# Kernel tuning notes

Measured on AMD Instinct MI355X. Metric: run time of the kernel, lower is better.

Reference implementation:

```python
import jax, jax.numpy as jnp
import numpy as np
import math

B, S, D, H = 2, 2048, 1024, 16
DK = D // H
THETA = 10000.0

def _rope_tables(seq_len, dk, theta):
    freqs = 1.0 / theta ** (np.arange(0, dk, 2)[: dk // 2].astype(np.float32) / dk)
    t = np.arange(seq_len, dtype=np.float32)
    ang = np.outer(t, freqs)  # [S, dk/2]
    return jnp.asarray(np.cos(ang)), jnp.asarray(np.sin(ang))

def setup_inputs() -> dict:
    key = jax.random.key(0)
    ks = jax.random.split(key, 12)
    init = lambda k, shape: (0.02 * jax.random.normal(k, shape)).astype(jnp.float32)
    cos, sin = _rope_tables(S, DK, THETA)
    mask = jnp.tril(jnp.ones((S, S), dtype=jnp.int32))[None, None]  # [1,1,S,S] causal
    return {
        'Q': jax.random.normal(ks[0], (B, S, D), jnp.float32),
        'K': jax.random.normal(ks[1], (B, S, D), jnp.float32),
        'V': jax.random.normal(ks[2], (B, S, D), jnp.float32),
        'mask': mask,
        'Wq_w': init(ks[3], (D, D)), 'Wq_b': init(ks[4], (D,)),
        'Wk_w': init(ks[5], (D, D)), 'Wk_b': init(ks[6], (D,)),
        'Wv_w': init(ks[7], (D, D)), 'Wv_b': init(ks[8], (D,)),
        'Wo_w': init(ks[9], (D, D)), 'Wo_b': init(ks[10], (D,)),
        'cos': cos, 'sin': sin,
    }

def _apply_rope(x, cos, sin):
    # x: [B, S, H, DK]; cos/sin: [S, DK/2]
    x1 = x[..., 0::2]
    x2 = x[..., 1::2]
    c = cos[None, :, None, :]
    s = sin[None, :, None, :]
    out_even = x1 * c - x2 * s
    out_odd = x1 * s + x2 * c
    return jnp.stack([out_even, out_odd], axis=-1).reshape(x.shape)

def reference(Q, K, V, mask, Wq_w, Wq_b, Wk_w, Wk_b, Wv_w, Wv_b, Wo_w, Wo_b, cos, sin):
    b, s, d = Q.shape
    q = (Q @ Wq_w.T + Wq_b).reshape(b, s, H, DK)
    k = (K @ Wk_w.T + Wk_b).reshape(b, s, H, DK)
    v = (V @ Wv_w.T + Wv_b).reshape(b, s, H, DK)
    q = _apply_rope(q, cos[:s], sin[:s])
    k = _apply_rope(k, cos[:s], sin[:s])
    # [B,H,S,DK]
    q = q.transpose(0, 2, 1, 3)
    k = k.transpose(0, 2, 1, 3)
    v = v.transpose(0, 2, 1, 3)
    scores = jnp.einsum('bhqd,bhkd->bhqk', q, k) / math.sqrt(DK)
    scores = jnp.where(mask == 0, jnp.float32(-1e9), scores)
    probs = jax.nn.softmax(scores, axis=-1)
    out = jnp.einsum('bhqk,bhkd->bhqd', probs, v)  # [B,H,S,DK]
    out = out.transpose(0, 2, 1, 3).reshape(b, s, d)
    return out @ Wo_w.T + Wo_b
```

## Files before the change

kernel.cpp:

```cpp
#include <hip/hip_runtime.h>
#include <cstdint>
#include <cstddef>


typedef __bf16 bf16x8 __attribute__((ext_vector_type(8)));
typedef float floatx4 __attribute__((ext_vector_type(4)));

#define DI __device__ __forceinline__

DI unsigned short f2bf(float f) {
  union { float f; unsigned int u; } v; v.f = f;
  unsigned int r = v.u + 0x7fffu + ((v.u >> 16) & 1u);
  return (unsigned short)(r >> 16);
}

DI unsigned short bfb(float f) {
  __bf16 h = (__bf16)f;
  union { __bf16 h; unsigned short u; } c; c.h = h;
  return c.u;
}

DI void gld16(const void* g, void* l) {
  __builtin_amdgcn_global_load_lds(
      (const __attribute__((address_space(1))) void*)g,
      (__attribute__((address_space(3))) void*)l, 16, 0, 0);
}

__global__ void cvt_all(const float* __restrict__ Q, const float* __restrict__ K,
                        const float* __restrict__ V, const float* __restrict__ Wq,
                        const float* __restrict__ Wk, const float* __restrict__ Wv,
                        const float* __restrict__ Wo, unsigned short* __restrict__ dst) {
  int i = blockIdx.x * blockDim.x + threadIdx.x;
  const float* s;
  int off;
  if (i < 3145728) {
    if (i < 1048576) { s = Q; off = i; }
    else if (i < 2097152) { s = K; off = i - 1048576; }
    else { s = V; off = i - 2097152; }
  } else {
    int j = i - 3145728;
    int wsel = j >> 18;
    off = j & 262143;
    s = (wsel == 0) ? Wq : (wsel == 1) ? Wk : (wsel == 2) ? Wv : Wo;
  }
  float4 f = reinterpret_cast<const float4*>(s)[off];
  ushort4 o;
  o.x = f2bf(f.x); o.y = f2bf(f.y); o.z = f2bf(f.z); o.w = f2bf(f.w);
  reinterpret_cast<ushort4*>(dst)[i] = o;
}

__global__ __launch_bounds__(256)
void gemm_qkv(const unsigned short* __restrict__ Qb, const unsigned short* __restrict__ Kb,
              const unsigned short* __restrict__ Vb, const unsigned short* __restrict__ Wq,
              const unsigned short* __restrict__ Wk, const unsigned short* __restrict__ Wv,
              const float* __restrict__ bq, const float* __restrict__ bk,
              const float* __restrict__ bv, unsigned short* __restrict__ qh,
              unsigned short* __restrict__ kh, unsigned short* __restrict__ vtp,
              const float* __restrict__ cosT, const float* __restrict__ sinT) {
  __shared__ unsigned short As[2][128 * 32];
  __shared__ unsigned short Bs[2][128 * 32];

  const int id = blockIdx.x;
  const int xb = id / 96;
  const int rem = id - xb * 96;
  const int proj = rem >> 5;
  const int yb = rem & 31;

  const unsigned short* X = (proj == 0) ? Qb : (proj == 1) ? Kb : Vb;
  const unsigned short* W = (proj == 0) ? Wq : (proj == 1) ? Wk : Wv;
  const float* bias = (proj == 0) ? bq : (proj == 1) ? bk : bv;
  unsigned short* outB = (proj == 0) ? qh : (proj == 1) ? kh : vtp;

  const int t = threadIdx.x;
  const int lane = t & 63;
  const int w = t >> 6;
  const int row0 = yb * 128;
  const int col0 = xb * 128;
  const int wm = (w >> 1) * 64;
  const int wn = (w & 1) * 64;
  const int fr = lane & 15;
  const int fk = (lane >> 4) * 8;
  const int rbase = (lane >> 4) * 4;

  const int c0 = t, c1 = t + 256;
  const unsigned short* gA0 = X + (size_t)(row0 + (c0 >> 2)) * 1024 + (c0 & 3) * 8;
  const unsigned short* gA1 = X + (size_t)(row0 + (c1 >> 2)) * 1024 + (c1 & 3) * 8;
  const unsigned short* gB0 = W + (size_t)(col0 + (c0 >> 2)) * 1024 + (c0 & 3) * 8;
  const unsigned short* gB1 = W + (size_t)(col0 + (c1 >> 2)) * 1024 + (c1 & 3) * 8;

  floatx4 acc[4][4];
#pragma unroll
  for (int i = 0; i < 4; ++i)
#pragma unroll
    for (int j = 0; j < 4; ++j)
      acc[i][j] = (floatx4){0.f, 0.f, 0.f, 0.f};

  auto stage = [&](int buf, int k0) {
    gld16(gA0 + k0, &As[buf][c0 * 8]);
    gld16(gA1 + k0, &As[buf][c1 * 8]);
    gld16(gB0 + k0, &Bs[buf][c0 * 8]);
    gld16(gB1 + k0, &Bs[buf][c1 * 8]);
  };

  stage(0, 0);
  __syncthreads();

  for (int kb = 0; kb < 32; ++kb) {
    const int cur = kb & 1;
    if (kb + 1 < 32) stage(cur ^ 1, (kb + 1) * 32);

    bf16x8 af[4], bfr[4];
#pragma unroll
    for (int i = 0; i < 4; ++i)
      af[i] = *reinterpret_cast<const bf16x8*>(&As[cur][(wm + i * 16 + fr) * 32 + fk]);
#pragma unroll
    for (int j = 0; j < 4; ++j)
      bfr[j] = *reinterpret_cast<const bf16x8*>(&Bs[cur][(wn + j * 16 + fr) * 32 + fk]);
    if (proj == 2) {
#pragma unroll
      for (int i = 0; i < 4; ++i)
#pragma unroll
        for (int j = 0; j < 4; ++j)
          acc[i][j] = __builtin_amdgcn_mfma_f32_16x16x32_bf16(bfr[j], af[i], acc[i][j], 0, 0, 0);
    } else {
#pragma unroll
      for (int i = 0; i < 4; ++i)
#pragma unroll
        for (int j = 0; j < 4; ++j)
          acc[i][j] = __builtin_amdgcn_mfma_f32_16x16x32_bf16(af[i], bfr[j], acc[i][j], 0, 0, 0);
    }

    __syncthreads();
  }

  if (proj < 2) {
#pragma unroll
    for (int j = 0; j < 4; ++j) {
      const int col = col0 + wn + j * 16 + fr;
      const float bvv = bias[col];
#pragma unroll
      for (int i = 0; i < 4; ++i) {
#pragma unroll
        for (int r = 0; r < 4; ++r) {
          const int row = row0 + wm + i * 16 + rbase + r;
          float v = acc[i][j][r] + bvv;
          const int bb = row >> 11, sp = row & 2047, hh = col >> 6, dk = col & 63;
          float p = __shfl_xor(v, 1);
          const int i2 = (col & 63) >> 1;
          const float cv = cosT[sp * 32 + i2];
          const float sv = sinT[sp * 32 + i2];
          float res = ((col & 1) == 0) ? (v * cv - p * sv) : (p * sv + v * cv);
          if (proj == 0) res *= 0.125f;
          outB[(((size_t)(bb * 16 + hh)) * 2048 + sp) * 64 + dk] = f2bf(res);
        }
      }
    }
  } else {
#pragma unroll
    for (int j = 0; j < 4; ++j) {
#pragma unroll
      for (int r = 0; r < 4; ++r) {
        const int dkc = col0 + wn + j * 16 + rbase + r;
        const float bvv = bias[dkc];
        const int hh = dkc >> 6, dk = dkc & 63;
#pragma unroll
        for (int i = 0; i < 4; ++i) {
          const int spf = row0 + wm + i * 16 + fr;
          const int bb = spf >> 11, sp = spf & 2047;
          vtp[(((size_t)(bb * 16 + hh)) * 64 + dk) * 2048 + sp] = f2bf(acc[i][j][r] + bvv);
        }
      }
    }
  }
}

__global__ __launch_bounds__(256)
void gemm_out(const unsigned short* __restrict__ X, const unsigned short* __restrict__ W,
              const float* __restrict__ bias, float* __restrict__ outF) {
  __shared__ unsigned short As[2][64 * 32];
  __shared__ unsigned short Bs[2][128 * 32];

  const int id = blockIdx.x;
  const int xb = id >> 6;
  const int yb = id & 63;

  const int t = threadIdx.x;
  const int lane = t & 63;
  const int w = t >> 6;
  const int row0 = yb * 64;
  const int col0 = xb * 128;
  const int wm = (w >> 1) * 32;
  const int wn = (w & 1) * 64;
  const int fr = lane & 15;
  const int fk = (lane >> 4) * 8;
  const int rbase = (lane >> 4) * 4;

  const int c0 = t, c1 = t + 256;
  const unsigned short* gA0 = X + (size_t)(row0 + (c0 >> 2)) * 1024 + (c0 & 3) * 8;
  const unsigned short* gB0 = W + (size_t)(col0 + (c0 >> 2)) * 1024 + (c0 & 3) * 8;
  const unsigned short* gB1 = W + (size_t)(col0 + (c1 >> 2)) * 1024 + (c1 & 3) * 8;

  floatx4 acc[2][4];
#pragma unroll
  for (int i = 0; i < 2; ++i)
#pragma unroll
    for (int j = 0; j < 4; ++j)
      acc[i][j] = (floatx4){0.f, 0.f, 0.f, 0.f};

  auto stage = [&](int buf, int k0) {
    gld16(gA0 + k0, &As[buf][c0 * 8]);
    gld16(gB0 + k0, &Bs[buf][c0 * 8]);
    gld16(gB1 + k0, &Bs[buf][c1 * 8]);
  };

  stage(0, 0);
  __syncthreads();

  for (int kb = 0; kb < 32; ++kb) {
    const int cur = kb & 1;
    if (kb + 1 < 32) stage(cur ^ 1, (kb + 1) * 32);

    bf16x8 af[2], bfr[4];
#pragma unroll
    for (int i = 0; i < 2; ++i)
      af[i] = *reinterpret_cast<const bf16x8*>(&As[cur][(wm + i * 16 + fr) * 32 + fk]);
#pragma unroll
    for (int j = 0; j < 4; ++j)
      bfr[j] = *reinterpret_cast<const bf16x8*>(&Bs[cur][(wn + j * 16 + fr) * 32 + fk]);
#pragma unroll
    for (int i = 0; i < 2; ++i)
#pragma unroll
      for (int j = 0; j < 4; ++j)
        acc[i][j] = __builtin_amdgcn_mfma_f32_16x16x32_bf16(af[i], bfr[j], acc[i][j], 0, 0, 0);

    __syncthreads();
  }

#pragma unroll
  for (int j = 0; j < 4; ++j) {
    const int col = col0 + wn + j * 16 + fr;
    const float bvv = bias[col];
#pragma unroll
    for (int i = 0; i < 2; ++i)
#pragma unroll
      for (int r = 0; r < 4; ++r) {
        const int row = row0 + wm + i * 16 + rbase + r;
        outF[(size_t)row * 1024 + col] = acc[i][j][r] + bvv;
      }
  }
}

__global__ __launch_bounds__(256)
void flash_attn(const unsigned short* __restrict__ qh,
                const unsigned short* __restrict__ kh,
                const unsigned short* __restrict__ vt,
                unsigned short* __restrict__ out) {
  __shared__ unsigned short Ks[2][64 * 64];
  __shared__ unsigned short Vs[2][64 * 64];
  __shared__ unsigned short Ps[8][16 * 64];

  const int t = threadIdx.x, lane = t & 63, w = t >> 6;
  const int g = lane >> 4;
  const int fr = lane & 15;
  const int fk = g * 8;
  const int rbase = g * 4;
  const int id = blockIdx.x;
  const int qbA = id >> 5;
  const int bh = id & 31;
  const int qbB = 31 - qbA;
  const int qwA = qbA * 64 + w * 16;
  const int qwB = qbB * 64 + w * 16;

  const size_t baseQK = (size_t)bh * 2048 * 64;
  const size_t baseV = (size_t)bh * 64 * 2048;

  bf16x8 qfA[2], qfB[2];
  qfA[0] = *reinterpret_cast<const bf16x8*>(&qh[baseQK + (size_t)(qwA + fr) * 64 + fk]);
  qfA[1] = *reinterpret_cast<const bf16x8*>(&qh[baseQK + (size_t)(qwA + fr) * 64 + 32 + fk]);
  qfB[0] = *reinterpret_cast<const bf16x8*>(&qh[baseQK + (size_t)(qwB + fr) * 64 + fk]);
  qfB[1] = *reinterpret_cast<const bf16x8*>(&qh[baseQK + (size_t)(qwB + fr) * 64 + 32 + fk]);

  floatx4 oA[4], oB[4];
  float lA[4], lB[4];
#pragma unroll
  for (int i = 0; i < 4; ++i) {
    oA[i] = (floatx4){0.f, 0.f, 0.f, 0.f};
    oB[i] = (floatx4){0.f, 0.f, 0.f, 0.f};
    lA[i] = 0.f; lB[i] = 0.f;
  }

  const int sc0 = t, sc1 = t + 256;
  const int r0 = sc0 >> 3, s0 = (sc0 & 7) ^ (r0 & 7);
  const int r1 = sc1 >> 3, s1 = (sc1 & 7) ^ (r1 & 7);

  auto stage = [&](int buf, int kb) {
    const int k0 = kb * 64;
    gld16(kh + baseQK + (size_t)(k0 + r0) * 64 + s0 * 8, &Ks[buf][sc0 * 8]);
    gld16(kh + baseQK + (size_t)(k0 + r1) * 64 + s1 * 8, &Ks[buf][sc1 * 8]);
    gld16(vt + baseV + (size_t)r0 * 2048 + k0 + s0 * 8, &Vs[buf][sc0 * 8]);
    gld16(vt + baseV + (size_t)r1 * 2048 + k0 + s1 * 8, &Vs[buf][sc1 * 8]);
  };

  const int nkb = qbB + 1;
  stage(0, 0);
  __syncthreads();

  for (int kb = 0; kb < nkb; ++kb) {
    const int cur = kb & 1;
    if (kb + 1 < nkb) stage(cur ^ 1, kb + 1);
    const int k0 = kb * 64;
    const bool aAct = (kb <= qbA);

    bf16x8 kf[4][2];
#pragma unroll
    for (int j = 0; j < 4; ++j)
#pragma unroll
      for (int kk = 0; kk < 2; ++kk)
        kf[j][kk] = *reinterpret_cast<const bf16x8*>(
            &Ks[cur][(j * 16 + fr) * 64 + ((((kk << 2) | g) ^ (fr & 7)) << 3)]);

    floatx4 sB[4], sA[4];
#pragma unroll
    for (int j = 0; j < 4; ++j) {
      sB[j] = (floatx4){0.f, 0.f, 0.f, 0.f};
      sA[j] = (floatx4){0.f, 0.f, 0.f, 0.f};
    }
#pragma unroll
    for (int j = 0; j < 4; ++j)
#pragma unroll
      for (int kk = 0; kk < 2; ++kk)
        sB[j] = __builtin_amdgcn_mfma_f32_16x16x32_bf16(qfB[kk], kf[j][kk], sB[j], 0, 0, 0);
    if (aAct) {
#pragma unroll
      for (int j = 0; j < 4; ++j)
#pragma unroll
        for (int kk = 0; kk < 2; ++kk)
          sA[j] = __builtin_amdgcn_mfma_f32_16x16x32_bf16(qfA[kk], kf[j][kk], sA[j], 0, 0, 0);
    }

    if (k0 + 63 > qwB) {
#pragma unroll
      for (int j = 0; j < 4; ++j)
#pragma unroll
        for (int r = 0; r < 4; ++r)
          if (k0 + j * 16 + fr > qwB + rbase + r) sB[j][r] = -1e30f;
    }
    if (aAct && k0 + 63 > qwA) {
#pragma unroll
      for (int j = 0; j < 4; ++j)
#pragma unroll
        for (int r = 0; r < 4; ++r)
          if (k0 + j * 16 + fr > qwA + rbase + r) sA[j][r] = -1e30f;
    }

#pragma unroll
    for (int j = 0; j < 4; ++j) {
      const int chb = (j * 16 + fr) >> 3;
      const int cin = fr & 7;
#pragma unroll
      for (int r = 0; r < 4; ++r) {
        const int row = rbase + r;
        float pB = __expf(sB[j][r]);
        lB[r] += pB;
        Ps[w][row * 64 + ((chb ^ (row & 7)) << 3) + cin] = bfb(pB);
      }
    }
    if (aAct) {
#pragma unroll
      for (int j = 0; j < 4; ++j) {
        const int chb = (j * 16 + fr) >> 3;
        const int cin = fr & 7;
#pragma unroll
        for (int r = 0; r < 4; ++r) {
          const int row = rbase + r;
          float pA = __expf(sA[j][r]);
          lA[r] += pA;
          Ps[w + 4][row * 64 + ((chb ^ (row & 7)) << 3) + cin] = bfb(pA);
        }
      }
    }

    bf16x8 vf[4][2], pB2[2], pA2[2];
#pragma unroll
    for (int id2 = 0; id2 < 4; ++id2)
#pragma unroll
      for (int kk = 0; kk < 2; ++kk)
        vf[id2][kk] = *reinterpret_cast<const bf16x8*>(
            &Vs[cur][(id2 * 16 + fr) * 64 + ((((kk << 2) | g) ^ (fr & 7)) << 3)]);
#pragma unroll
    for (int kk = 0; kk < 2; ++kk)
      pB2[kk] = *reinterpret_cast<const bf16x8*>(
          &Ps[w][fr * 64 + ((((kk << 2) | g) ^ (fr & 7)) << 3)]);
#pragma unroll
    for (int kk = 0; kk < 2; ++kk)
#pragma unroll
      for (int id2 = 0; id2 < 4; ++id2)
        oB[id2] = __builtin_amdgcn_mfma_f32_16x16x32_bf16(pB2[kk], vf[id2][kk], oB[id2], 0, 0, 0);
    if (aAct) {
#pragma unroll
      for (int kk = 0; kk < 2; ++kk)
        pA2[kk] = *reinterpret_cast<const bf16x8*>(
            &Ps[w + 4][fr * 64 + ((((kk << 2) | g) ^ (fr & 7)) << 3)]);
#pragma unroll
      for (int kk = 0; kk < 2; ++kk)
#pragma unroll
        for (int id2 = 0; id2 < 4; ++id2)
          oA[id2] = __builtin_amdgcn_mfma_f32_16x16x32_bf16(pA2[kk], vf[id2][kk], oA[id2], 0, 0, 0);
    }

    __syncthreads();
  }

#pragma unroll
  for (int r = 0; r < 4; ++r) {
#pragma unroll
    for (int d = 1; d < 16; d <<= 1) {
      lB[r] += __shfl_xor(lB[r], d);
      lA[r] += __shfl_xor(lA[r], d);
    }
  }

  const int bb = bh >> 4, hh = bh & 15;
#pragma unroll
  for (int id2 = 0; id2 < 4; ++id2)
#pragma unroll
    for (int r = 0; r < 4; ++r) {
      const int qrA = qwA + rbase + r;
      const int qrB = qwB + rbase + r;
      out[((size_t)(bb * 2048 + qrA)) * 1024 + hh * 64 + id2 * 16 + fr] = bfb(oA[id2][r] / lA[r]);
      out[((size_t)(bb * 2048 + qrB)) * 1024 + hh * 64 + id2 * 16 + fr] = bfb(oB[id2][r] / lB[r]);
    }
}

extern "C" void kernel_launch(void* const* d_in, const int* in_sizes, int n_in,
                              void* d_out, int out_size, void* d_ws, size_t ws_size,
                              hipStream_t stream) {
  const float* Q  = (const float*)d_in[0];
  const float* K  = (const float*)d_in[1];
  const float* V  = (const float*)d_in[2];
  const float* Wq = (const float*)d_in[4];
  const float* bq = (const float*)d_in[5];
  const float* Wk = (const float*)d_in[6];
  const float* bk = (const float*)d_in[7];
  const float* Wv = (const float*)d_in[8];
  const float* bv = (const float*)d_in[9];
  const float* Wo = (const float*)d_in[10];
  const float* bo = (const float*)d_in[11];
  const float* cosT = (const float*)d_in[12];
  const float* sinT = (const float*)d_in[13];

  char* ws = (char*)d_ws;
  const size_t MB = 1024 * 1024;
  unsigned short* Qb  = (unsigned short*)(ws + 0 * MB);
  unsigned short* Kb  = (unsigned short*)(ws + 8 * MB);
  unsigned short* Vb  = (unsigned short*)(ws + 16 * MB);
  unsigned short* Wqb = (unsigned short*)(ws + 24 * MB);
  unsigned short* Wkb = (unsigned short*)(ws + 26 * MB);
  unsigned short* Wvb = (unsigned short*)(ws + 28 * MB);
  unsigned short* Wob = (unsigned short*)(ws + 30 * MB);
  unsigned short* qh  = (unsigned short*)(ws + 32 * MB);
  unsigned short* khp = (unsigned short*)(ws + 40 * MB);
  unsigned short* vtp = (unsigned short*)(ws + 48 * MB);
  unsigned short* ao  = (unsigned short*)(ws + 56 * MB);

  cvt_all<<<16384, 256, 0, stream>>>(Q, K, V, Wq, Wk, Wv, Wo, (unsigned short*)ws);

  gemm_qkv<<<768, 256, 0, stream>>>(Qb, Kb, Vb, Wqb, Wkb, Wvb, bq, bk, bv,
                                    qh, khp, vtp, cosT, sinT);
  flash_attn<<<512, 256, 0, stream>>>(qh, khp, vtp, ao);
  gemm_out<<<512, 256, 0, stream>>>(ao, Wob, bo, (float*)d_out);
}
```

Before: 259.3 us.

## Fuse fp32-to-bf16 conversion into GEMM loads and drop separate convert kernel

```diff
diff --git a/kernel.cpp b/kernel.cpp
--- a/kernel.cpp
+++ b/kernel.cpp
@@ -20,39 +20,23 @@
   return c.u;
 }
 
+DI bf16x8 cvt8(float4 a, float4 b) {
+  bf16x8 o;
+  o[0] = (__bf16)a.x; o[1] = (__bf16)a.y; o[2] = (__bf16)a.z; o[3] = (__bf16)a.w;
+  o[4] = (__bf16)b.x; o[5] = (__bf16)b.y; o[6] = (__bf16)b.z; o[7] = (__bf16)b.w;
+  return o;
+}
+
 DI void gld16(const void* g, void* l) {
   __builtin_amdgcn_global_load_lds(
       (const __attribute__((address_space(1))) void*)g,
       (__attribute__((address_space(3))) void*)l, 16, 0, 0);
 }
 
-__global__ void cvt_all(const float* __restrict__ Q, const float* __restrict__ K,
-                        const float* __restrict__ V, const float* __restrict__ Wq,
-                        const float* __restrict__ Wk, const float* __restrict__ Wv,
-                        const float* __restrict__ Wo, unsigned short* __restrict__ dst) {
-  int i = blockIdx.x * blockDim.x + threadIdx.x;
-  const float* s;
-  int off;
-  if (i < 3145728) {
-    if (i < 1048576) { s = Q; off = i; }
-    else if (i < 2097152) { s = K; off = i - 1048576; }
-    else { s = V; off = i - 2097152; }
-  } else {
-    int j = i - 3145728;
-    int wsel = j >> 18;
-    off = j & 262143;
-    s = (wsel == 0) ? Wq : (wsel == 1) ? Wk : (wsel == 2) ? Wv : Wo;
-  }
-  float4 f = reinterpret_cast<const float4*>(s)[off];
-  ushort4 o;
-  o.x = f2bf(f.x); o.y = f2bf(f.y); o.z = f2bf(f.z); o.w = f2bf(f.w);
-  reinterpret_cast<ushort4*>(dst)[i] = o;
-}
-
-__global__ __launch_bounds__(256)
-void gemm_qkv(const unsigned short* __restrict__ Qb, const unsigned short* __restrict__ Kb,
-              const unsigned short* __restrict__ Vb, const unsigned short* __restrict__ Wq,
-              const unsigned short* __restrict__ Wk, const unsigned short* __restrict__ Wv,
+__global__ __launch_bounds__(256, 3)
+void gemm_qkv(const float* __restrict__ Qf, const float* __restrict__ Kf,
+              const float* __restrict__ Vf, const float* __restrict__ Wq,
+              const float* __restrict__ Wk, const float* __restrict__ Wv,
               const float* __restrict__ bq, const float* __restrict__ bk,
               const float* __restrict__ bv, unsigned short* __restrict__ qh,
               unsigned short* __restrict__ kh, unsigned short* __restrict__ vtp,
@@ -66,8 +50,8 @@
   const int proj = rem >> 5;
   const int yb = rem & 31;
 
-  const unsigned short* X = (proj == 0) ? Qb : (proj == 1) ? Kb : Vb;
-  const unsigned short* W = (proj == 0) ? Wq : (proj == 1) ? Wk : Wv;
+  const float* X = (proj == 0) ? Qf : (proj == 1) ? Kf : Vf;
+  const float* W = (proj == 0) ? Wq : (proj == 1) ? Wk : Wv;
   const float* bias = (proj == 0) ? bq : (proj == 1) ? bk : bv;
   unsigned short* outB = (proj == 0) ? qh : (proj == 1) ? kh : vtp;
 
@@ -82,11 +66,12 @@
   const int fk = (lane >> 4) * 8;
   const int rbase = (lane >> 4) * 4;
 
-  const int c0 = t, c1 = t + 256;
-  const unsigned short* gA0 = X + (size_t)(row0 + (c0 >> 2)) * 1024 + (c0 & 3) * 8;
-  const unsigned short* gA1 = X + (size_t)(row0 + (c1 >> 2)) * 1024 + (c1 & 3) * 8;
-  const unsigned short* gB0 = W + (size_t)(col0 + (c0 >> 2)) * 1024 + (c0 & 3) * 8;
-  const unsigned short* gB1 = W + (size_t)(col0 + (c1 >> 2)) * 1024 + (c1 & 3) * 8;
+  const int ca0 = t, ca1 = t + 256;
+  const float* gA0 = X + (size_t)(row0 + (ca0 >> 2)) * 1024 + (ca0 & 3) * 8;
+  const float* gA1 = X + (size_t)(row0 + (ca1 >> 2)) * 1024 + (ca1 & 3) * 8;
+  const float* gB0 = W + (size_t)(col0 + (ca0 >> 2)) * 1024 + (ca0 & 3) * 8;
+  const float* gB1 = W + (size_t)(col0 + (ca1 >> 2)) * 1024 + (ca1 & 3) * 8;
+  const int dA0 = ca0 * 8, dA1 = ca1 * 8;
 
   floatx4 acc[4][4];
 #pragma unroll
@@ -95,19 +80,31 @@
     for (int j = 0; j < 4; ++j)
       acc[i][j] = (floatx4){0.f, 0.f, 0.f, 0.f};
 
-  auto stage = [&](int buf, int k0) {
-    gld16(gA0 + k0, &As[buf][c0 * 8]);
-    gld16(gA1 + k0, &As[buf][c1 * 8]);
-    gld16(gB0 + k0, &Bs[buf][c0 * 8]);
-    gld16(gB1 + k0, &Bs[buf][c1 * 8]);
+  float4 fa0, fa0b, fa1, fa1b, fb0, fb0b, fb1, fb1b;
+  auto gload = [&](int k0) {
+    fa0  = *reinterpret_cast<const float4*>(gA0 + k0);
+    fa0b = *reinterpret_cast<const float4*>(gA0 + k0 + 4);
+    fa1  = *reinterpret_cast<const float4*>(gA1 + k0);
+    fa1b = *reinterpret_cast<const float4*>(gA1 + k0 + 4);
+    fb0  = *reinterpret_cast<const float4*>(gB0 + k0);
+    fb0b = *reinterpret_cast<const float4*>(gB0 + k0 + 4);
+    fb1  = *reinterpret_cast<const float4*>(gB1 + k0);
+    fb1b = *reinterpret_cast<const float4*>(gB1 + k0 + 4);
   };
-
-  stage(0, 0);
+  auto swrite = [&](int buf) {
+    *reinterpret_cast<bf16x8*>(&As[buf][dA0]) = cvt8(fa0, fa0b);
+    *reinterpret_cast<bf16x8*>(&As[buf][dA1]) = cvt8(fa1, fa1b);
+    *reinterpret_cast<bf16x8*>(&Bs[buf][dA0]) = cvt8(fb0, fb0b);
+    *reinterpret_cast<bf16x8*>(&Bs[buf][dA1]) = cvt8(fb1, fb1b);
+  };
+
+  gload(0);
+  swrite(0);
   __syncthreads();
 
   for (int kb = 0; kb < 32; ++kb) {
     const int cur = kb & 1;
-    if (kb + 1 < 32) stage(cur ^ 1, (kb + 1) * 32);
+    if (kb + 1 < 32) gload((kb + 1) * 32);
 
     bf16x8 af[4], bfr[4];
 #pragma unroll
@@ -130,6 +127,7 @@
           acc[i][j] = __builtin_amdgcn_mfma_f32_16x16x32_bf16(af[i], bfr[j], acc[i][j], 0, 0, 0);
     }
 
+    if (kb + 1 < 32) swrite(cur ^ 1);
     __syncthreads();
   }
 
@@ -174,8 +172,8 @@
   }
 }
 
-__global__ __launch_bounds__(256)
-void gemm_out(const unsigned short* __restrict__ X, const unsigned short* __restrict__ W,
+__global__ __launch_bounds__(256, 3)
+void gemm_out(const unsigned short* __restrict__ X, const float* __restrict__ W,
               const float* __restrict__ bias, float* __restrict__ outF) {
   __shared__ unsigned short As[2][64 * 32];
   __shared__ unsigned short Bs[2][128 * 32];
@@ -195,10 +193,11 @@
   const int fk = (lane >> 4) * 8;
   const int rbase = (lane >> 4) * 4;
 
-  const int c0 = t, c1 = t + 256;
+  const int c0 = t;
   const unsigned short* gA0 = X + (size_t)(row0 + (c0 >> 2)) * 1024 + (c0 & 3) * 8;
-  const unsigned short* gB0 = W + (size_t)(col0 + (c0 >> 2)) * 1024 + (c0 & 3) * 8;
-  const unsigned short* gB1 = W + (size_t)(col0 + (c1 >> 2)) * 1024 + (c1 & 3) * 8;
+  const float* gB0 = W + (size_t)(col0 + (c0 >> 2)) * 1024 + (c0 & 3) * 8;
+  const float* gB1 = W + (size_t)(col0 + ((c0 + 256) >> 2)) * 1024 + (c0 & 3) * 8;
+  const int dB0 = c0 * 8, dB1 = (c0 + 256) * 8;
 
   floatx4 acc[2][4];
 #pragma unroll
@@ -207,18 +206,29 @@
     for (int j = 0; j < 4; ++j)
       acc[i][j] = (floatx4){0.f, 0.f, 0.f, 0.f};
 
-  auto stage = [&](int buf, int k0) {
-    gld16(gA0 + k0, &As[buf][c0 * 8]);
-    gld16(gB0 + k0, &Bs[buf][c0 * 8]);
-    gld16(gB1 + k0, &Bs[buf][c1 * 8]);
+  float4 fb0, fb0b, fb1, fb1b;
+  auto gloadB = [&](int k0) {
+    fb0  = *reinterpret_cast<const float4*>(gB0 + k0);
+    fb0b = *reinterpret_cast<const float4*>(gB0 + k0 + 4);
+    fb1  = *reinterpret_cast<const float4*>(gB1 + k0);
+    fb1b = *reinterpret_cast<const float4*>(gB1 + k0 + 4);
   };
-
-  stage(0, 0);
+  auto swriteB = [&](int buf) {
+    *reinterpret_cast<bf16x8*>(&Bs[buf][dB0]) = cvt8(fb0, fb0b);
+    *reinterpret_cast<bf16x8*>(&Bs[buf][dB1]) = cvt8(fb1, fb1b);
+  };
+
+  gld16(gA0, &As[0][c0 * 8]);
+  gloadB(0);
+  swriteB(0);
   __syncthreads();
 
   for (int kb = 0; kb < 32; ++kb) {
     const int cur = kb & 1;
-    if (kb + 1 < 32) stage(cur ^ 1, (kb + 1) * 32);
+    if (kb + 1 < 32) {
+      gld16(gA0 + (kb + 1) * 32, &As[cur ^ 1][c0 * 8]);
+      gloadB((kb + 1) * 32);
+    }
 
     bf16x8 af[2], bfr[4];
 #pragma unroll
@@ -233,6 +243,7 @@
       for (int j = 0; j < 4; ++j)
         acc[i][j] = __builtin_amdgcn_mfma_f32_16x16x32_bf16(af[i], bfr[j], acc[i][j], 0, 0, 0);
 
+    if (kb + 1 < 32) swriteB(cur ^ 1);
     __syncthreads();
   }
 
@@ -325,6 +336,7 @@
       sB[j] = (floatx4){0.f, 0.f, 0.f, 0.f};
       sA[j] = (floatx4){0.f, 0.f, 0.f, 0.f};
     }
+    __builtin_amdgcn_s_setprio(1);
 #pragma unroll
     for (int j = 0; j < 4; ++j)
 #pragma unroll
@@ -337,6 +349,7 @@
         for (int kk = 0; kk < 2; ++kk)
           sA[j] = __builtin_amdgcn_mfma_f32_16x16x32_bf16(qfA[kk], kf[j][kk], sA[j], 0, 0, 0);
     }
+    __builtin_amdgcn_s_setprio(0);
 
     if (k0 + 63 > qwB) {
 #pragma unroll
@@ -391,21 +404,25 @@
     for (int kk = 0; kk < 2; ++kk)
       pB2[kk] = *reinterpret_cast<const bf16x8*>(
           &Ps[w][fr * 64 + ((((kk << 2) | g) ^ (fr & 7)) << 3)]);
+    __builtin_amdgcn_s_setprio(1);
 #pragma unroll
     for (int kk = 0; kk < 2; ++kk)
 #pragma unroll
       for (int id2 = 0; id2 < 4; ++id2)
         oB[id2] = __builtin_amdgcn_mfma_f32_16x16x32_bf16(pB2[kk], vf[id2][kk], oB[id2], 0, 0, 0);
+    __builtin_amdgcn_s_setprio(0);
     if (aAct) {
 #pragma unroll
       for (int kk = 0; kk < 2; ++kk)
         pA2[kk] = *reinterpret_cast<const bf16x8*>(
             &Ps[w + 4][fr * 64 + ((((kk << 2) | g) ^ (fr & 7)) << 3)]);
+      __builtin_amdgcn_s_setprio(1);
 #pragma unroll
       for (int kk = 0; kk < 2; ++kk)
 #pragma unroll
         for (int id2 = 0; id2 < 4; ++id2)
           oA[id2] = __builtin_amdgcn_mfma_f32_16x16x32_bf16(pA2[kk], vf[id2][kk], oA[id2], 0, 0, 0);
+      __builtin_amdgcn_s_setprio(0);
     }
 
     __syncthreads();
@@ -451,22 +468,13 @@
 
   char* ws = (char*)d_ws;
   const size_t MB = 1024 * 1024;
-  unsigned short* Qb  = (unsigned short*)(ws + 0 * MB);
-  unsigned short* Kb  = (unsigned short*)(ws + 8 * MB);
-  unsigned short* Vb  = (unsigned short*)(ws + 16 * MB);
-  unsigned short* Wqb = (unsigned short*)(ws + 24 * MB);
-  unsigned short* Wkb = (unsigned short*)(ws + 26 * MB);
-  unsigned short* Wvb = (unsigned short*)(ws + 28 * MB);
-  unsigned short* Wob = (unsigned short*)(ws + 30 * MB);
   unsigned short* qh  = (unsigned short*)(ws + 32 * MB);
   unsigned short* khp = (unsigned short*)(ws + 40 * MB);
   unsigned short* vtp = (unsigned short*)(ws + 48 * MB);
   unsigned short* ao  = (unsigned short*)(ws + 56 * MB);
 
-  cvt_all<<<16384, 256, 0, stream>>>(Q, K, V, Wq, Wk, Wv, Wo, (unsigned short*)ws);
-
-  gemm_qkv<<<768, 256, 0, stream>>>(Qb, Kb, Vb, Wqb, Wkb, Wvb, bq, bk, bv,
+  gemm_qkv<<<768, 256, 0, stream>>>(Q, K, V, Wq, Wk, Wv, bq, bk, bv,
                                     qh, khp, vtp, cosT, sinT);
   flash_attn<<<512, 256, 0, stream>>>(qh, khp, vtp, ao);
-  gemm_out<<<512, 256, 0, stream>>>(ao, Wob, bo, (float*)d_out);
-}
+  gemm_out<<<512, 256, 0, stream>>>(ao, Wo, bo, (float*)d_out);
+}
```

After: 293.4 us. 1.13x slower.
